# Performance work log

Hardware: AMD Instinct MI355X
Metric: run time of the kernel (lower is better)

The kernel has to match this reference:

```python
import jax, jax.numpy as jnp
import numpy as np

B, L, D_MODEL = 1, 1024, 768
H = 12            # num_heads == num_key_value_heads
FDIM = 16         # feature_dim
HEAD_DIM = D_MODEL // H  # 64
EPS = 1e-12
R2 = np.sqrt(2.0)
RD = np.sqrt(float(FDIM))        # sqrt(16) = 4
RRD = np.sqrt(RD)                # sqrt(4) = 2


def setup_inputs() -> dict:
    key = jax.random.key(0)
    ks = jax.random.split(key, 5)
    s = 1.0 / np.sqrt(D_MODEL)
    return {
        "hidden_states": jax.random.normal(ks[0], (B, L, D_MODEL), dtype=jnp.float32),
        "Wq": jax.random.normal(ks[1], (D_MODEL, H * FDIM), dtype=jnp.float32) * s,
        "Wk": jax.random.normal(ks[2], (D_MODEL, H * FDIM), dtype=jnp.float32) * s,
        "Wv": jax.random.normal(ks[3], (D_MODEL, D_MODEL), dtype=jnp.float32) * s,
        "Wo": jax.random.normal(ks[4], (D_MODEL, D_MODEL), dtype=jnp.float32) * s,
    }


def taylor_exp_feature_map(x):
    # x: (b, h, l, FDIM) -> (b, h, l, 1 + FDIM + FDIM^2)
    x2 = (x[..., :, None] * x[..., None, :]).reshape(*x.shape[:-1], FDIM * FDIM) / R2
    ones = jnp.ones((*x.shape[:-1], 1), dtype=x.dtype)
    return jnp.concatenate([ones, x / RRD, x2 / RD], axis=-1)


def reference(hidden_states, Wq, Wk, Wv, Wo):
    b, l, _ = hidden_states.shape
    q = (hidden_states @ Wq).reshape(b, l, H, FDIM).transpose(0, 2, 1, 3)
    k = (hidden_states @ Wk).reshape(b, l, H, FDIM).transpose(0, 2, 1, 3)
    v = (hidden_states @ Wv).reshape(b, l, H, HEAD_DIM).transpose(0, 2, 1, 3)
    q = taylor_exp_feature_map(q)  # (b,h,l,Dexp)
    k = taylor_exp_feature_map(k)  # (b,h,l,Dexp)
    # causal linear attention: y_t = q_t . cumsum_t(k_s v_s^T) / (q_t . cumsum_t(k_s) + eps)
    kv = k[..., :, None] * v[..., None, :]          # (b,h,l,Dexp,hd)
    kv_cum = jnp.cumsum(kv, axis=2)                  # (b,h,l,Dexp,hd)
    num = jnp.einsum('bhln,bhlnd->bhld', q, kv_cum)  # (b,h,l,hd)
    k_cum = jnp.cumsum(k, axis=2)                    # (b,h,l,Dexp)
    den = jnp.einsum('bhln,bhln->bhl', q, k_cum)[..., None] + EPS
    y = num / den                                    # (b,h,l,hd)
    y = y.transpose(0, 2, 1, 3).reshape(b, l, H * HEAD_DIM)
    return y @ Wo
```

## Files before the change

### kernel.cpp

```cpp
#include <hip/hip_runtime.h>

#define C2 0.17677669529663687f

typedef __attribute__((ext_vector_type(8))) short short8;
typedef __attribute__((ext_vector_type(8))) unsigned short ushort8;
typedef __attribute__((ext_vector_type(4))) float f32x4;

__device__ __forceinline__ unsigned short f2bf(float x) {
    union { float f; unsigned u; } v; v.f = x;
    unsigned r = v.u + 0x7fffu + ((v.u >> 16) & 1u);
    return (unsigned short)(r >> 16);
}
__device__ __forceinline__ float bf2f(unsigned short u) {
    union { unsigned u; float f; } v; v.u = ((unsigned)u) << 16;
    return v.f;
}

__device__ __forceinline__ void gemm_inblk_splitk(
    const float* __restrict__ A, const float* __restrict__ W,
    float* __restrict__ out, int row0, int n0, int outcol0, int ldw, int outld)
{
    __shared__ unsigned short Al[2][2][64][40];
    __shared__ unsigned short Bl[2][2][64][40];
    __shared__ float red[64][65];
    const int tid = threadIdx.x;
    const int g = tid >> 8;
    const int t = tid & 255;
    const int lane = t & 63, wave4 = t >> 6;
    const int wm = wave4 & 1, wn = wave4 >> 1;
    const int quad = lane >> 4, lr = lane & 15;
    const int k0base = g * 384;

    f32x4 acc[2][2] = {{{0.f,0.f,0.f,0.f},{0.f,0.f,0.f,0.f}},
                       {{0.f,0.f,0.f,0.f},{0.f,0.f,0.f,0.f}}};

    float4 ra[2], rb[2];
    #pragma unroll
    for (int l = 0; l < 2; ++l) {
        int idx = t + l * 256;
        ra[l] = *(const float4*)&A[(size_t)(row0 + (idx >> 3)) * 768 + k0base + (idx & 7) * 4];
        rb[l] = *(const float4*)&W[(size_t)(k0base + (idx >> 4)) * ldw + n0 + (idx & 15) * 4];
    }
    #pragma unroll
    for (int l = 0; l < 2; ++l) {
        int idx = t + l * 256;
        *(ushort4*)&Al[g][0][idx >> 3][(idx & 7) * 4] =
            make_ushort4(f2bf(ra[l].x), f2bf(ra[l].y), f2bf(ra[l].z), f2bf(ra[l].w));
        int kr = idx >> 4, nq = (idx & 15) * 4;
        int col = (((kr >> 3) ^ ((idx & 15) >> 2)) << 3) | (kr & 7);
        Bl[g][0][nq + 0][col] = f2bf(rb[l].x);
        Bl[g][0][nq + 1][col] = f2bf(rb[l].y);
        Bl[g][0][nq + 2][col] = f2bf(rb[l].z);
        Bl[g][0][nq + 3][col] = f2bf(rb[l].w);
    }
    __syncthreads();

    const int ITER = 12;
    #pragma unroll
    for (int i = 0; i < ITER; ++i) {
        const int cur = i & 1, nxt = cur ^ 1;
        float4 na[2], nb[2];
        if (i + 1 < ITER) {
            int kn = k0base + (i + 1) * 32;
            #pragma unroll
            for (int l = 0; l < 2; ++l) {
                int idx = t + l * 256;
                na[l] = *(const float4*)&A[(size_t)(row0 + (idx >> 3)) * 768 + kn + (idx & 7) * 4];
                nb[l] = *(const float4*)&W[(size_t)(kn + (idx >> 4)) * ldw + n0 + (idx & 15) * 4];
            }
        }
        short8 af[2], bfr[2];
        #pragma unroll
        for (int mi = 0; mi < 2; ++mi)
            af[mi] = *(const short8*)&Al[g][cur][wm * 32 + mi * 16 + lr][quad << 3];
        #pragma unroll
        for (int ni = 0; ni < 2; ++ni) {
            int csw = quad ^ ((wn * 2 + ni) & 3);
            bfr[ni] = *(const short8*)&Bl[g][cur][wn * 32 + ni * 16 + lr][csw << 3];
        }
        #pragma unroll
        for (int mi = 0; mi < 2; ++mi)
            #pragma unroll
            for (int ni = 0; ni < 2; ++ni)
                acc[mi][ni] = __builtin_amdgcn_mfma_f32_16x16x32_bf16(af[mi], bfr[ni], acc[mi][ni], 0, 0, 0);
        if (i + 1 < ITER) {
            #pragma unroll
            for (int l = 0; l < 2; ++l) {
                int idx = t + l * 256;
                *(ushort4*)&Al[g][nxt][idx >> 3][(idx & 7) * 4] =
                    make_ushort4(f2bf(na[l].x), f2bf(na[l].y), f2bf(na[l].z), f2bf(na[l].w));
                int kr = idx >> 4, nq = (idx & 15) * 4;
                int col = (((kr >> 3) ^ ((idx & 15) >> 2)) << 3) | (kr & 7);
                Bl[g][nxt][nq + 0][col] = f2bf(nb[l].x);
                Bl[g][nxt][nq + 1][col] = f2bf(nb[l].y);
                Bl[g][nxt][nq + 2][col] = f2bf(nb[l].z);
                Bl[g][nxt][nq + 3][col] = f2bf(nb[l].w);
            }
        }
        __syncthreads();
    }
    if (g == 1) {
        #pragma unroll
        for (int mi = 0; mi < 2; ++mi)
            #pragma unroll
            for (int ni = 0; ni < 2; ++ni)
                #pragma unroll
                for (int r = 0; r < 4; ++r)
                    red[wm * 32 + mi * 16 + quad * 4 + r][wn * 32 + ni * 16 + lr] = acc[mi][ni][r];
    }
    __syncthreads();
    if (g == 0) {
        #pragma unroll
        for (int mi = 0; mi < 2; ++mi)
            #pragma unroll
            for (int ni = 0; ni < 2; ++ni)
                #pragma unroll
                for (int r = 0; r < 4; ++r) {
                    int rr = wm * 32 + mi * 16 + quad * 4 + r;
                    int cc = wn * 32 + ni * 16 + lr;
                    out[(size_t)(row0 + rr) * outld + outcol0 + cc] = acc[mi][ni][r] + red[rr][cc];
                }
    }
}

__global__ __launch_bounds__(512) void gemm_qkv_mfma(
    const float* __restrict__ H, const float* __restrict__ Wq,
    const float* __restrict__ Wk, const float* __restrict__ Wv,
    float* __restrict__ out)
{
    const int nt = blockIdx.x, mt = blockIdx.y;
    const float* W; int ldw, n0;
    if (nt < 3)      { W = Wq; ldw = 192; n0 = nt * 64; }
    else if (nt < 6) { W = Wk; ldw = 192; n0 = (nt - 3) * 64; }
    else             { W = Wv; ldw = 768; n0 = (nt - 6) * 64; }
    gemm_inblk_splitk(H, W, out, mt * 64, n0, nt * 64, ldw, 1152);
}

__global__ __launch_bounds__(512) void gemm_wo_mfma(
    const float* __restrict__ Y, const float* __restrict__ Wo, float* __restrict__ out)
{
    const int nt = blockIdx.x, mt = blockIdx.y;
    gemm_inblk_splitk(Y, Wo, out, mt * 64, nt * 64, nt * 64, 768, 768);
}

__global__ __launch_bounds__(256) void chunk_state_k(
    const float* __restrict__ qkv, unsigned short* __restrict__ St, float* __restrict__ z)
{
    const int c = blockIdx.x, h = blockIdx.y;
    __shared__ float Kc[64][17];
    __shared__ unsigned short Pk[320][72];
    __shared__ unsigned short Vt[80][72];
    const int tid = threadIdx.x;
    const int lane = tid & 63, wave = tid >> 6;
    const int quad = lane >> 4, lr = lane & 15;

    {
        int s = tid >> 2, f4 = (tid & 3) * 4;
        float4 kv = *(const float4*)&qkv[(size_t)(c * 64 + s) * 1152 + 192 + h * 16 + f4];
        Kc[s][f4 + 0] = kv.x; Kc[s][f4 + 1] = kv.y; Kc[s][f4 + 2] = kv.z; Kc[s][f4 + 3] = kv.w;
    }
    #pragma unroll
    for (int l = 0; l < 4; ++l) {
        int idx = tid + l * 256;
        int s = idx >> 4, d4 = (idx & 15) * 4;
        float4 vv = *(const float4*)&qkv[(size_t)(c * 64 + s) * 1152 + 384 + h * 64 + d4];
        Vt[d4 + 0][s] = f2bf(vv.x);
        Vt[d4 + 1][s] = f2bf(vv.y);
        Vt[d4 + 2][s] = f2bf(vv.z);
        Vt[d4 + 3][s] = f2bf(vv.w);
    }
    for (int idx = tid; idx < 16 * 72; idx += 256) {
        int rr = 64 + idx / 72, ss = idx % 72;
        Vt[rr][ss] = (rr == 64 && ss < 64) ? (unsigned short)0x3F80 : (unsigned short)0;
    }
    __syncthreads();
    for (int idx = tid; idx < 2880; idx += 256) {
        int n = idx / 9, s8 = (idx % 9) * 8;
        short8 v8;
        #pragma unroll
        for (int tt = 0; tt < 8; ++tt) {
            int s = s8 + tt;
            float ph = 0.f;
            if (s < 64 && n < 273) {
                if (n == 0) ph = 1.f;
                else if (n < 17) ph = Kc[s][n - 1] * 0.5f;
                else { int m = n - 17; ph = Kc[s][m >> 4] * Kc[s][m & 15] * C2; }
            }
            v8[tt] = (short)f2bf(ph);
        }
        *(short8*)&Pk[n][s8] = v8;
    }
    __syncthreads();

    f32x4 acc[5][5];
    #pragma unroll
    for (int a = 0; a < 5; ++a)
        #pragma unroll
        for (int b = 0; b < 5; ++b) acc[a][b] = (f32x4){0.f, 0.f, 0.f, 0.f};
    #pragma unroll
    for (int ks = 0; ks < 2; ++ks) {
        short8 af[5], bfr[5];
        #pragma unroll
        for (int mt = 0; mt < 5; ++mt)
            af[mt] = *(const short8*)&Vt[mt * 16 + lr][ks * 32 + quad * 8];
        #pragma unroll
        for (int nt = 0; nt < 5; ++nt)
            bfr[nt] = *(const short8*)&Pk[(wave * 5 + nt) * 16 + lr][ks * 32 + quad * 8];
        #pragma unroll
        for (int mt = 0; mt < 5; ++mt)
            #pragma unroll
            for (int nt = 0; nt < 5; ++nt)
                acc[mt][nt] = __builtin_amdgcn_mfma_f32_16x16x32_bf16(af[mt], bfr[nt], acc[mt][nt], 0, 0, 0);
    }
    unsigned short* Sbt = St + (size_t)(h * 16 + c) * 18432;
    float* zb = z + (h * 16 + c) * 273;
    #pragma unroll
    for (int nt = 0; nt < 5; ++nt) {
        int n = (wave * 5 + nt) * 16 + lr;
        if (n < 273) {
            #pragma unroll
            for (int mt = 0; mt < 4; ++mt)
                #pragma unroll
                for (int r = 0; r < 4; ++r)
                    Sbt[(mt * 16 + quad * 4 + r) * 288 + n] = f2bf(acc[mt][nt][r]);
            if (quad == 0) zb[n] = acc[4][nt][0];
        }
    }
}

__global__ __launch_bounds__(256) void scan_state_k(unsigned short* __restrict__ St, float* __restrict__ z)
{
    const int NS = 12 * 64 * 273;
    int e = blockIdx.x * 256 + threadIdx.x;
    if (e < NS) {
        int hh = e / (64 * 273), rem = e % (64 * 273);
        int d = rem / 273, n = rem % 273;
        unsigned short* p = St + (size_t)hh * 16 * 18432 + d * 288 + n;
        float run = 0.f;
        #pragma unroll
        for (int c = 0; c < 16; ++c) {
            float v = bf2f(p[c * 18432]);
            p[c * 18432] = f2bf(run);
            run += v;
        }
    } else if (e < NS + 12 * 273) {
        int e2 = e - NS, hh = e2 / 273, n = e2 % 273;
        float* p = z + hh * 16 * 273 + n;
        float run = 0.f;
        #pragma unroll
        for (int c = 0; c < 16; ++c) { float v = p[c * 273]; p[c * 273] = run; run += v; }
    }
}

__global__ __launch_bounds__(256) void chunk_out_k(
    const float* __restrict__ qkv, const unsigned short* __restrict__ St, const float* __restrict__ z,
    float* __restrict__ y)
{
    const int c = blockIdx.x, h = blockIdx.y;
    __shared__ float Qc[64][17];
    __shared__ unsigned short Aq[64][40];
    __shared__ unsigned short Kb[64][40];
    __shared__ unsigned short Pq[64][360];
    __shared__ unsigned short Sv[64][360];
    __shared__ float zl[288];
    __shared__ float dpart[6][64];
    const int tid = threadIdx.x;
    const int lane = tid & 63, wave = tid >> 6;
    const int wm = wave & 1, wn = wave >> 1;
    const int quad = lane >> 4, lr = lane & 15;

    {
        int s = tid >> 2, f4 = (tid & 3) * 4;
        const float* base = &qkv[(size_t)(c * 64 + s) * 1152 + h * 16];
        float4 qv = *(const float4*)&base[f4];
        float4 kv = *(const float4*)&base[192 + f4];
        Qc[s][f4 + 0] = qv.x; Qc[s][f4 + 1] = qv.y; Qc[s][f4 + 2] = qv.z; Qc[s][f4 + 3] = qv.w;
        *(ushort4*)&Aq[s][f4] = make_ushort4(f2bf(qv.x), f2bf(qv.y), f2bf(qv.z), f2bf(qv.w));
        *(ushort4*)&Kb[s][f4] = make_ushort4(f2bf(kv.x), f2bf(kv.y), f2bf(kv.z), f2bf(kv.w));
        *(ushort4*)&Aq[s][16 + (tid & 3) * 4] = make_ushort4(0, 0, 0, 0);
        *(ushort4*)&Kb[s][16 + (tid & 3) * 4] = make_ushort4(0, 0, 0, 0);
    }
    #pragma unroll
    for (int l = 0; l < 4; ++l) {
        int idx = tid + l * 256;
        int s = idx >> 4, d4 = (idx & 15) * 4;
        float4 vv = *(const float4*)&qkv[(size_t)(c * 64 + s) * 1152 + 384 + h * 64 + d4];
        Sv[d4 + 0][288 + s] = f2bf(vv.x);
        Sv[d4 + 1][288 + s] = f2bf(vv.y);
        Sv[d4 + 2][288 + s] = f2bf(vv.z);
        Sv[d4 + 3][288 + s] = f2bf(vv.w);
    }
    const unsigned short* Sgt = St + (size_t)(h * 16 + c) * 18432;
    for (int idx = tid; idx < 64 * 34; idx += 256) {
        int d = idx / 34, n8 = (idx % 34) * 8;
        *(ushort8*)&Sv[d][n8] = *(const ushort8*)&Sgt[d * 288 + n8];
    }
    for (int idx = tid; idx < 64; idx += 256) Sv[idx][272] = Sgt[idx * 288 + 272];
    for (int idx = tid; idx < 64 * 15; idx += 256) {
        int d = idx / 15, n = 273 + idx % 15;
        Sv[d][n] = 0;
    }
    const float* zg = z + (h * 16 + c) * 273;
    for (int idx = tid; idx < 288; idx += 256) zl[idx] = (idx < 273) ? zg[idx] : 0.f;
    __syncthreads();

    f32x4 accS[2][2] = {{{0.f,0.f,0.f,0.f},{0.f,0.f,0.f,0.f}},
                        {{0.f,0.f,0.f,0.f},{0.f,0.f,0.f,0.f}}};
    {
        short8 af[2], bfr[2];
        #pragma unroll
        for (int mi = 0; mi < 2; ++mi)
            af[mi] = *(const short8*)&Aq[wm * 32 + mi * 16 + lr][quad * 8];
        #pragma unroll
        for (int ni = 0; ni < 2; ++ni)
            bfr[ni] = *(const short8*)&Kb[wn * 32 + ni * 16 + lr][quad * 8];
        #pragma unroll
        for (int mi = 0; mi < 2; ++mi)
            #pragma unroll
            for (int ni = 0; ni < 2; ++ni)
                accS[mi][ni] = __builtin_amdgcn_mfma_f32_16x16x32_bf16(af[mi], bfr[ni], accS[mi][ni], 0, 0, 0);
    }

    {
        int i = lane;
        float qr[16];
        #pragma unroll
        for (int f = 0; f < 16; ++f) qr[f] = Qc[i][f];
        float dp = 0.f;
        int n0 = wave * 72;
        for (int n = n0; n < n0 + 72; ++n) {
            float ph;
            if (n == 0) ph = 1.f;
            else if (n < 17) ph = qr[n - 1] * 0.5f;
            else if (n < 273) { int m = n - 17; ph = qr[m >> 4] * qr[m & 15] * C2; }
            else ph = 0.f;
            Pq[i][n] = f2bf(ph);
            dp += ph * zl[n];
        }
        dpart[wave][i] = dp;
    }

    #pragma unroll
    for (int mi = 0; mi < 2; ++mi) {
        float rs[4] = {0.f, 0.f, 0.f, 0.f};
        #pragma unroll
        for (int ni = 0; ni < 2; ++ni)
            #pragma unroll
            for (int r = 0; r < 4; ++r) {
                int i = wm * 32 + mi * 16 + quad * 4 + r;
                int j = wn * 32 + ni * 16 + lr;
                float u = accS[mi][ni][r];
                float sc = (j <= i) ? (1.f + 0.25f * u + u * u * (1.f / 32.f)) : 0.f;
                rs[r] += sc;
                Pq[i][288 + j] = f2bf(sc);
            }
        #pragma unroll
        for (int r = 0; r < 4; ++r) {
            float v = rs[r];
            v += __shfl_xor(v, 1);
            v += __shfl_xor(v, 2);
            v += __shfl_xor(v, 4);
            v += __shfl_xor(v, 8);
            if (lr == 0) dpart[4 + wn][wm * 32 + mi * 16 + quad * 4 + r] = v;
        }
    }
    __syncthreads();

    f32x4 acc[2][2] = {{{0.f,0.f,0.f,0.f},{0.f,0.f,0.f,0.f}},
                       {{0.f,0.f,0.f,0.f},{0.f,0.f,0.f,0.f}}};
    #pragma unroll
    for (int ks = 0; ks < 11; ++ks) {
        short8 af[2], bfr[2];
        #pragma unroll
        for (int mi = 0; mi < 2; ++mi)
            af[mi] = *(const short8*)&Pq[wm * 32 + mi * 16 + lr][ks * 32 + quad * 8];
        #pragma unroll
        for (int ni = 0; ni < 2; ++ni)
            bfr[ni] = *(const short8*)&Sv[wn * 32 + ni * 16 + lr][ks * 32 + quad * 8];
        #pragma unroll
        for (int mi = 0; mi < 2; ++mi)
            #pragma unroll
            for (int ni = 0; ni < 2; ++ni)
                acc[mi][ni] = __builtin_amdgcn_mfma_f32_16x16x32_bf16(af[mi], bfr[ni], acc[mi][ni], 0, 0, 0);
    }

    #pragma unroll
    for (int mi = 0; mi < 2; ++mi)
        #pragma unroll
        for (int r = 0; r < 4; ++r) {
            int i = wm * 32 + mi * 16 + quad * 4 + r;
            float den = dpart[0][i] + dpart[1][i] + dpart[2][i] +
                        dpart[3][i] + dpart[4][i] + dpart[5][i] + 1e-12f;
            float rden = 1.f / den;
            #pragma unroll
            for (int ni = 0; ni < 2; ++ni)
                y[(size_t)(c * 64 + i) * 768 + h * 64 + wn * 32 + ni * 16 + lr] = acc[mi][ni][r] * rden;
        }
}

extern "C" void kernel_launch(void* const* d_in, const int* in_sizes, int n_in,
                              void* d_out, int out_size, void* d_ws, size_t ws_size,
                              hipStream_t stream) {
    const float* hs = (const float*)d_in[0];
    const float* Wq = (const float*)d_in[1];
    const float* Wk = (const float*)d_in[2];
    const float* Wv = (const float*)d_in[3];
    const float* Wo = (const float*)d_in[4];
    float* out = (float*)d_out;
    float* ws  = (float*)d_ws;

    float* qkv = ws;
    float* yb  = ws + 1179648;
    unsigned short* St = (unsigned short*)(ws + 1966080);
    float* zb  = ws + 5320704;

    gemm_qkv_mfma<<<dim3(18, 16), 512, 0, stream>>>(hs, Wq, Wk, Wv, qkv);
    chunk_state_k<<<dim3(16, 12), 256, 0, stream>>>(qkv, St, zb);
    scan_state_k <<<832, 256, 0, stream>>>(St, zb);
    chunk_out_k  <<<dim3(16, 12), 256, 0, stream>>>(qkv, St, zb, yb);
    gemm_wo_mfma <<<dim3(12, 16), 512, 0, stream>>>(yb, Wo, out);
}
```

Measured before the change: 137.6 us.

## Fuse five kernels into one persistent kernel with software grid barriers

Replaces the five separate launches (QKV GEMM, chunk state, scan, chunk output, Wo GEMM) with a single 192-block persistent kernel. Phases are separated by an atomic-counter grid barrier, and shared memory is overlaid through a union. The goal is to remove launch gaps and inter-kernel drain. In exchange, the QKV GEMM is spread unevenly across blocks (some do two tiles), the chunk-state MFMA work is redistributed across 8 waves, and a memset is added per call. The grid barrier only works if all 192 blocks are co-resident.

```diff
diff --git a/kernel.cpp b/kernel.cpp
--- a/kernel.cpp
+++ b/kernel.cpp
@@ -16,13 +16,52 @@
     return v.f;
 }
 
-__device__ __forceinline__ void gemm_inblk_splitk(
-    const float* __restrict__ A, const float* __restrict__ W,
+struct SplitKSm {
+    unsigned short Al[2][2][64][40];
+    unsigned short Bl[2][2][64][40];
+    float red[64][65];
+};
+struct StateSm {
+    float Kc[64][17];
+    unsigned short Pk[320][72];
+    unsigned short Vt[80][72];
+};
+struct OutSm {
+    float Qc[64][17];
+    unsigned short Aq[64][40];
+    unsigned short Kb[64][40];
+    unsigned short Pq[64][360];
+    unsigned short Sv[64][360];
+    float zl[288];
+    float dpart[6][64];
+};
+union __align__(16) SmemU { SplitKSm g; StateSm a; OutSm c; };
+
+__device__ __forceinline__ void grid_sync(int* bar, int nblk) {
+    __syncthreads();
+    if (threadIdx.x == 0) {
+        __threadfence();
+        int gen = __hip_atomic_load(&bar[1], __ATOMIC_RELAXED, __HIP_MEMORY_SCOPE_AGENT);
+        int arr = __hip_atomic_fetch_add(&bar[0], 1, __ATOMIC_ACQ_REL, __HIP_MEMORY_SCOPE_AGENT);
+        if (arr == nblk - 1) {
+            __hip_atomic_store(&bar[0], 0, __ATOMIC_RELAXED, __HIP_MEMORY_SCOPE_AGENT);
+            __hip_atomic_store(&bar[1], gen + 1, __ATOMIC_RELEASE, __HIP_MEMORY_SCOPE_AGENT);
+        } else {
+            int cur;
+            do {
+                __builtin_amdgcn_s_sleep(2);
+                cur = __hip_atomic_load(&bar[1], __ATOMIC_ACQUIRE, __HIP_MEMORY_SCOPE_AGENT);
+            } while (cur == gen);
+        }
+        __threadfence();
+    }
+    __syncthreads();
+}
+
+__device__ void gemm_inblk_splitk(
+    SplitKSm& smem, const float* __restrict__ A, const float* __restrict__ W,
     float* __restrict__ out, int row0, int n0, int outcol0, int ldw, int outld)
 {
-    __shared__ unsigned short Al[2][2][64][40];
-    __shared__ unsigned short Bl[2][2][64][40];
-    __shared__ float red[64][65];
     const int tid = threadIdx.x;
     const int g = tid >> 8;
     const int t = tid & 255;
@@ -44,14 +83,14 @@
     #pragma unroll
     for (int l = 0; l < 2; ++l) {
         int idx = t + l * 256;
-        *(ushort4*)&Al[g][0][idx >> 3][(idx & 7) * 4] =
+        *(ushort4*)&smem.Al[g][0][idx >> 3][(idx & 7) * 4] =
             make_ushort4(f2bf(ra[l].x), f2bf(ra[l].y), f2bf(ra[l].z), f2bf(ra[l].w));
         int kr = idx >> 4, nq = (idx & 15) * 4;
         int col = (((kr >> 3) ^ ((idx & 15) >> 2)) << 3) | (kr & 7);
-        Bl[g][0][nq + 0][col] = f2bf(rb[l].x);
-        Bl[g][0][nq + 1][col] = f2bf(rb[l].y);
-        Bl[g][0][nq + 2][col] = f2bf(rb[l].z);
-        Bl[g][0][nq + 3][col] = f2bf(rb[l].w);
+        smem.Bl[g][0][nq + 0][col] = f2bf(rb[l].x);
+        smem.Bl[g][0][nq + 1][col] = f2bf(rb[l].y);
+        smem.Bl[g][0][nq + 2][col] = f2bf(rb[l].z);
+        smem.Bl[g][0][nq + 3][col] = f2bf(rb[l].w);
     }
     __syncthreads();
 
@@ -72,11 +111,11 @@
         short8 af[2], bfr[2];
         #pragma unroll
         for (int mi = 0; mi < 2; ++mi)
-            af[mi] = *(const short8*)&Al[g][cur][wm * 32 + mi * 16 + lr][quad << 3];
+            af[mi] = *(const short8*)&smem.Al[g][cur][wm * 32 + mi * 16 + lr][quad << 3];
         #pragma unroll
         for (int ni = 0; ni < 2; ++ni) {
             int csw = quad ^ ((wn * 2 + ni) & 3);
-            bfr[ni] = *(const short8*)&Bl[g][cur][wn * 32 + ni * 16 + lr][csw << 3];
+            bfr[ni] = *(const short8*)&smem.Bl[g][cur][wn * 32 + ni * 16 + lr][csw << 3];
         }
         #pragma unroll
         for (int mi = 0; mi < 2; ++mi)
@@ -87,14 +126,14 @@
             #pragma unroll
             for (int l = 0; l < 2; ++l) {
                 int idx = t + l * 256;
-                *(ushort4*)&Al[g][nxt][idx >> 3][(idx & 7) * 4] =
+                *(ushort4*)&smem.Al[g][nxt][idx >> 3][(idx & 7) * 4] =
                     make_ushort4(f2bf(na[l].x), f2bf(na[l].y), f2bf(na[l].z), f2bf(na[l].w));
                 int kr = idx >> 4, nq = (idx & 15) * 4;
                 int col = (((kr >> 3) ^ ((idx & 15) >> 2)) << 3) | (kr & 7);
-                Bl[g][nxt][nq + 0][col] = f2bf(nb[l].x);
-                Bl[g][nxt][nq + 1][col] = f2bf(nb[l].y);
-                Bl[g][nxt][nq + 2][col] = f2bf(nb[l].z);
-                Bl[g][nxt][nq + 3][col] = f2bf(nb[l].w);
+                smem.Bl[g][nxt][nq + 0][col] = f2bf(nb[l].x);
+                smem.Bl[g][nxt][nq + 1][col] = f2bf(nb[l].y);
+                smem.Bl[g][nxt][nq + 2][col] = f2bf(nb[l].z);
+                smem.Bl[g][nxt][nq + 3][col] = f2bf(nb[l].w);
             }
         }
         __syncthreads();
@@ -106,7 +145,7 @@
             for (int ni = 0; ni < 2; ++ni)
                 #pragma unroll
                 for (int r = 0; r < 4; ++r)
-                    red[wm * 32 + mi * 16 + quad * 4 + r][wn * 32 + ni * 16 + lr] = acc[mi][ni][r];
+                    smem.red[wm * 32 + mi * 16 + quad * 4 + r][wn * 32 + ni * 16 + lr] = acc[mi][ni][r];
     }
     __syncthreads();
     if (g == 0) {
@@ -118,284 +157,295 @@
                 for (int r = 0; r < 4; ++r) {
                     int rr = wm * 32 + mi * 16 + quad * 4 + r;
                     int cc = wn * 32 + ni * 16 + lr;
-                    out[(size_t)(row0 + rr) * outld + outcol0 + cc] = acc[mi][ni][r] + red[rr][cc];
-                }
-    }
-}
-
-__global__ __launch_bounds__(512) void gemm_qkv_mfma(
-    const float* __restrict__ H, const float* __restrict__ Wq,
-    const float* __restrict__ Wk, const float* __restrict__ Wv,
-    float* __restrict__ out)
+                    out[(size_t)(row0 + rr) * outld + outcol0 + cc] = acc[mi][ni][r] + smem.red[rr][cc];
+                }
+    }
+}
+
+__global__ __launch_bounds__(512) void based_mega(
+    const float* __restrict__ hs, const float* __restrict__ Wq, const float* __restrict__ Wk,
+    const float* __restrict__ Wv, const float* __restrict__ Wo, float* __restrict__ out,
+    float* __restrict__ qkv, float* __restrict__ yb, unsigned short* __restrict__ St,
+    float* __restrict__ zb, int* __restrict__ bar)
 {
-    const int nt = blockIdx.x, mt = blockIdx.y;
-    const float* W; int ldw, n0;
-    if (nt < 3)      { W = Wq; ldw = 192; n0 = nt * 64; }
-    else if (nt < 6) { W = Wk; ldw = 192; n0 = (nt - 3) * 64; }
-    else             { W = Wv; ldw = 768; n0 = (nt - 6) * 64; }
-    gemm_inblk_splitk(H, W, out, mt * 64, n0, nt * 64, ldw, 1152);
-}
-
-__global__ __launch_bounds__(512) void gemm_wo_mfma(
-    const float* __restrict__ Y, const float* __restrict__ Wo, float* __restrict__ out)
-{
-    const int nt = blockIdx.x, mt = blockIdx.y;
-    gemm_inblk_splitk(Y, Wo, out, mt * 64, nt * 64, nt * 64, 768, 768);
-}
-
-__global__ __launch_bounds__(256) void chunk_state_k(
-    const float* __restrict__ qkv, unsigned short* __restrict__ St, float* __restrict__ z)
-{
-    const int c = blockIdx.x, h = blockIdx.y;
-    __shared__ float Kc[64][17];
-    __shared__ unsigned short Pk[320][72];
-    __shared__ unsigned short Vt[80][72];
+    __shared__ SmemU sm;
+    const int b = blockIdx.x;
     const int tid = threadIdx.x;
-    const int lane = tid & 63, wave = tid >> 6;
-    const int quad = lane >> 4, lr = lane & 15;
 
     {
-        int s = tid >> 2, f4 = (tid & 3) * 4;
-        float4 kv = *(const float4*)&qkv[(size_t)(c * 64 + s) * 1152 + 192 + h * 16 + f4];
-        Kc[s][f4 + 0] = kv.x; Kc[s][f4 + 1] = kv.y; Kc[s][f4 + 2] = kv.z; Kc[s][f4 + 3] = kv.w;
-    }
-    #pragma unroll
-    for (int l = 0; l < 4; ++l) {
-        int idx = tid + l * 256;
-        int s = idx >> 4, d4 = (idx & 15) * 4;
-        float4 vv = *(const float4*)&qkv[(size_t)(c * 64 + s) * 1152 + 384 + h * 64 + d4];
-        Vt[d4 + 0][s] = f2bf(vv.x);
-        Vt[d4 + 1][s] = f2bf(vv.y);
-        Vt[d4 + 2][s] = f2bf(vv.z);
-        Vt[d4 + 3][s] = f2bf(vv.w);
-    }
-    for (int idx = tid; idx < 16 * 72; idx += 256) {
-        int rr = 64 + idx / 72, ss = idx % 72;
-        Vt[rr][ss] = (rr == 64 && ss < 64) ? (unsigned short)0x3F80 : (unsigned short)0;
-    }
-    __syncthreads();
-    for (int idx = tid; idx < 2880; idx += 256) {
-        int n = idx / 9, s8 = (idx % 9) * 8;
-        short8 v8;
-        #pragma unroll
-        for (int tt = 0; tt < 8; ++tt) {
-            int s = s8 + tt;
-            float ph = 0.f;
-            if (s < 64 && n < 273) {
-                if (n == 0) ph = 1.f;
-                else if (n < 17) ph = Kc[s][n - 1] * 0.5f;
-                else { int m = n - 17; ph = Kc[s][m >> 4] * Kc[s][m & 15] * C2; }
-            }
-            v8[tt] = (short)f2bf(ph);
-        }
-        *(short8*)&Pk[n][s8] = v8;
-    }
-    __syncthreads();
-
-    f32x4 acc[5][5];
-    #pragma unroll
-    for (int a = 0; a < 5; ++a)
-        #pragma unroll
-        for (int b = 0; b < 5; ++b) acc[a][b] = (f32x4){0.f, 0.f, 0.f, 0.f};
-    #pragma unroll
-    for (int ks = 0; ks < 2; ++ks) {
-        short8 af[5], bfr[5];
+        const int ntiles = (b < 96) ? 2 : 1;
+        for (int ti = 0; ti < ntiles; ++ti) {
+            int tl = b + ti * 192;
+            int mt = tl / 18, nt = tl % 18;
+            const float* W; int ldw, n0;
+            if (nt < 3)      { W = Wq; ldw = 192; n0 = nt * 64; }
+            else if (nt < 6) { W = Wk; ldw = 192; n0 = (nt - 3) * 64; }
+            else             { W = Wv; ldw = 768; n0 = (nt - 6) * 64; }
+            gemm_inblk_splitk(sm.g, hs, W, qkv, mt * 64, n0, nt * 64, ldw, 1152);
+        }
+    }
+    grid_sync(bar, 192);
+
+    const int c = b & 15, h = b >> 4;
+
+    {
+        if (tid < 256) {
+            int s = tid >> 2, f4 = (tid & 3) * 4;
+            float4 kv = *(const float4*)&qkv[(size_t)(c * 64 + s) * 1152 + 192 + h * 16 + f4];
+            sm.a.Kc[s][f4 + 0] = kv.x; sm.a.Kc[s][f4 + 1] = kv.y;
+            sm.a.Kc[s][f4 + 2] = kv.z; sm.a.Kc[s][f4 + 3] = kv.w;
+        }
+        #pragma unroll
+        for (int l = 0; l < 2; ++l) {
+            int idx = tid + l * 512;
+            int s = idx >> 4, d4 = (idx & 15) * 4;
+            float4 vv = *(const float4*)&qkv[(size_t)(c * 64 + s) * 1152 + 384 + h * 64 + d4];
+            sm.a.Vt[d4 + 0][s] = f2bf(vv.x);
+            sm.a.Vt[d4 + 1][s] = f2bf(vv.y);
+            sm.a.Vt[d4 + 2][s] = f2bf(vv.z);
+            sm.a.Vt[d4 + 3][s] = f2bf(vv.w);
+        }
+        for (int idx = tid; idx < 16 * 72; idx += 512) {
+            int rr = 64 + idx / 72, ss = idx % 72;
+            sm.a.Vt[rr][ss] = (rr == 64 && ss < 64) ? (unsigned short)0x3F80 : (unsigned short)0;
+        }
+        __syncthreads();
+        for (int idx = tid; idx < 2880; idx += 512) {
+            int n = idx / 9, s8 = (idx % 9) * 8;
+            short8 v8;
+            #pragma unroll
+            for (int tt = 0; tt < 8; ++tt) {
+                int s = s8 + tt;
+                float ph = 0.f;
+                if (s < 64 && n < 273) {
+                    if (n == 0) ph = 1.f;
+                    else if (n < 17) ph = sm.a.Kc[s][n - 1] * 0.5f;
+                    else { int m = n - 17; ph = sm.a.Kc[s][m >> 4] * sm.a.Kc[s][m & 15] * C2; }
+                }
+                v8[tt] = (short)f2bf(ph);
+            }
+            *(short8*)&sm.a.Pk[n][s8] = v8;
+        }
+        __syncthreads();
+
+        const int lane = tid & 63, wave = tid >> 6;
+        const int quad = lane >> 4, lr = lane & 15;
+        f32x4 acc[5][3];
         #pragma unroll
         for (int mt = 0; mt < 5; ++mt)
-            af[mt] = *(const short8*)&Vt[mt * 16 + lr][ks * 32 + quad * 8];
-        #pragma unroll
-        for (int nt = 0; nt < 5; ++nt)
-            bfr[nt] = *(const short8*)&Pk[(wave * 5 + nt) * 16 + lr][ks * 32 + quad * 8];
-        #pragma unroll
-        for (int mt = 0; mt < 5; ++mt)
-            #pragma unroll
-            for (int nt = 0; nt < 5; ++nt)
-                acc[mt][nt] = __builtin_amdgcn_mfma_f32_16x16x32_bf16(af[mt], bfr[nt], acc[mt][nt], 0, 0, 0);
-    }
-    unsigned short* Sbt = St + (size_t)(h * 16 + c) * 18432;
-    float* zb = z + (h * 16 + c) * 273;
-    #pragma unroll
-    for (int nt = 0; nt < 5; ++nt) {
-        int n = (wave * 5 + nt) * 16 + lr;
-        if (n < 273) {
-            #pragma unroll
-            for (int mt = 0; mt < 4; ++mt)
-                #pragma unroll
-                for (int r = 0; r < 4; ++r)
-                    Sbt[(mt * 16 + quad * 4 + r) * 288 + n] = f2bf(acc[mt][nt][r]);
-            if (quad == 0) zb[n] = acc[4][nt][0];
-        }
-    }
-}
-
-__global__ __launch_bounds__(256) void scan_state_k(unsigned short* __restrict__ St, float* __restrict__ z)
-{
-    const int NS = 12 * 64 * 273;
-    int e = blockIdx.x * 256 + threadIdx.x;
-    if (e < NS) {
-        int hh = e / (64 * 273), rem = e % (64 * 273);
-        int d = rem / 273, n = rem % 273;
-        unsigned short* p = St + (size_t)hh * 16 * 18432 + d * 288 + n;
-        float run = 0.f;
-        #pragma unroll
-        for (int c = 0; c < 16; ++c) {
-            float v = bf2f(p[c * 18432]);
-            p[c * 18432] = f2bf(run);
-            run += v;
-        }
-    } else if (e < NS + 12 * 273) {
-        int e2 = e - NS, hh = e2 / 273, n = e2 % 273;
-        float* p = z + hh * 16 * 273 + n;
-        float run = 0.f;
-        #pragma unroll
-        for (int c = 0; c < 16; ++c) { float v = p[c * 273]; p[c * 273] = run; run += v; }
-    }
-}
-
-__global__ __launch_bounds__(256) void chunk_out_k(
-    const float* __restrict__ qkv, const unsigned short* __restrict__ St, const float* __restrict__ z,
-    float* __restrict__ y)
-{
-    const int c = blockIdx.x, h = blockIdx.y;
-    __shared__ float Qc[64][17];
-    __shared__ unsigned short Aq[64][40];
-    __shared__ unsigned short Kb[64][40];
-    __shared__ unsigned short Pq[64][360];
-    __shared__ unsigned short Sv[64][360];
-    __shared__ float zl[288];
-    __shared__ float dpart[6][64];
-    const int tid = threadIdx.x;
-    const int lane = tid & 63, wave = tid >> 6;
-    const int wm = wave & 1, wn = wave >> 1;
-    const int quad = lane >> 4, lr = lane & 15;
+            #pragma unroll
+            for (int nt = 0; nt < 3; ++nt) acc[mt][nt] = (f32x4){0.f, 0.f, 0.f, 0.f};
+        #pragma unroll
+        for (int ks = 0; ks < 2; ++ks) {
+            short8 af[5], bfr[3];
+            #pragma unroll
+            for (int mt = 0; mt < 5; ++mt)
+                af[mt] = *(const short8*)&sm.a.Vt[mt * 16 + lr][ks * 32 + quad * 8];
+            #pragma unroll
+            for (int nt = 0; nt < 3; ++nt)
+                if (wave + 8 * nt < 20)
+                    bfr[nt] = *(const short8*)&sm.a.Pk[(wave + 8 * nt) * 16 + lr][ks * 32 + quad * 8];
+            #pragma unroll
+            for (int mt = 0; mt < 5; ++mt)
+                #pragma unroll
+                for (int nt = 0; nt < 3; ++nt)
+                    if (wave + 8 * nt < 20)
+                        acc[mt][nt] = __builtin_amdgcn_mfma_f32_16x16x32_bf16(af[mt], bfr[nt], acc[mt][nt], 0, 0, 0);
+        }
+        unsigned short* Sbt = St + (size_t)(h * 16 + c) * 18432;
+        float* zp = zb + (h * 16 + c) * 273;
+        #pragma unroll
+        for (int nt = 0; nt < 3; ++nt) {
+            if (wave + 8 * nt < 20) {
+                int n = (wave + 8 * nt) * 16 + lr;
+                if (n < 273) {
+                    #pragma unroll
+                    for (int mt = 0; mt < 4; ++mt)
+                        #pragma unroll
+                        for (int r = 0; r < 4; ++r)
+                            Sbt[(mt * 16 + quad * 4 + r) * 288 + n] = f2bf(acc[mt][nt][r]);
+                    if (quad == 0) zp[n] = acc[4][nt][0];
+                }
+            }
+        }
+    }
+    grid_sync(bar, 192);
 
     {
-        int s = tid >> 2, f4 = (tid & 3) * 4;
-        const float* base = &qkv[(size_t)(c * 64 + s) * 1152 + h * 16];
-        float4 qv = *(const float4*)&base[f4];
-        float4 kv = *(const float4*)&base[192 + f4];
-        Qc[s][f4 + 0] = qv.x; Qc[s][f4 + 1] = qv.y; Qc[s][f4 + 2] = qv.z; Qc[s][f4 + 3] = qv.w;
-        *(ushort4*)&Aq[s][f4] = make_ushort4(f2bf(qv.x), f2bf(qv.y), f2bf(qv.z), f2bf(qv.w));
-        *(ushort4*)&Kb[s][f4] = make_ushort4(f2bf(kv.x), f2bf(kv.y), f2bf(kv.z), f2bf(kv.w));
-        *(ushort4*)&Aq[s][16 + (tid & 3) * 4] = make_ushort4(0, 0, 0, 0);
-        *(ushort4*)&Kb[s][16 + (tid & 3) * 4] = make_ushort4(0, 0, 0, 0);
-    }
-    #pragma unroll
-    for (int l = 0; l < 4; ++l) {
-        int idx = tid + l * 256;
-        int s = idx >> 4, d4 = (idx & 15) * 4;
-        float4 vv = *(const float4*)&qkv[(size_t)(c * 64 + s) * 1152 + 384 + h * 64 + d4];
-        Sv[d4 + 0][288 + s] = f2bf(vv.x);
-        Sv[d4 + 1][288 + s] = f2bf(vv.y);
-        Sv[d4 + 2][288 + s] = f2bf(vv.z);
-        Sv[d4 + 3][288 + s] = f2bf(vv.w);
-    }
-    const unsigned short* Sgt = St + (size_t)(h * 16 + c) * 18432;
-    for (int idx = tid; idx < 64 * 34; idx += 256) {
-        int d = idx / 34, n8 = (idx % 34) * 8;
-        *(ushort8*)&Sv[d][n8] = *(const ushort8*)&Sgt[d * 288 + n8];
-    }
-    for (int idx = tid; idx < 64; idx += 256) Sv[idx][272] = Sgt[idx * 288 + 272];
-    for (int idx = tid; idx < 64 * 15; idx += 256) {
-        int d = idx / 15, n = 273 + idx % 15;
-        Sv[d][n] = 0;
-    }
-    const float* zg = z + (h * 16 + c) * 273;
-    for (int idx = tid; idx < 288; idx += 256) zl[idx] = (idx < 273) ? zg[idx] : 0.f;
-    __syncthreads();
-
-    f32x4 accS[2][2] = {{{0.f,0.f,0.f,0.f},{0.f,0.f,0.f,0.f}},
-                        {{0.f,0.f,0.f,0.f},{0.f,0.f,0.f,0.f}}};
+        int gid = b * 512 + tid;
+        const int NV = 12 * 64 * 36;
+        if (gid < NV) {
+            int hh = gid / (64 * 36), rem = gid % (64 * 36);
+            int d = rem / 36, nb = rem % 36;
+            unsigned short* p = St + (size_t)hh * 16 * 18432 + d * 288 + nb * 8;
+            ushort8 v[16];
+            #pragma unroll
+            for (int cc = 0; cc < 16; ++cc) v[cc] = *(const ushort8*)(p + (size_t)cc * 18432);
+            float run[8] = {0.f,0.f,0.f,0.f,0.f,0.f,0.f,0.f};
+            #pragma unroll
+            for (int cc = 0; cc < 16; ++cc) {
+                ushort8 w;
+                #pragma unroll
+                for (int j = 0; j < 8; ++j) {
+                    w[j] = f2bf(run[j]);
+                    run[j] += bf2f(v[cc][j]);
+                }
+                *(ushort8*)(p + (size_t)cc * 18432) = w;
+            }
+        } else if (gid < NV + 12 * 273) {
+            int e2 = gid - NV, hh = e2 / 273, n = e2 % 273;
+            float* p = zb + hh * 16 * 273 + n;
+            float v[16];
+            #pragma unroll
+            for (int cc = 0; cc < 16; ++cc) v[cc] = p[cc * 273];
+            float run = 0.f;
+            #pragma unroll
+            for (int cc = 0; cc < 16; ++cc) { p[cc * 273] = run; run += v[cc]; }
+        }
+    }
+    grid_sync(bar, 192);
+
     {
-        short8 af[2], bfr[2];
-        #pragma unroll
-        for (int mi = 0; mi < 2; ++mi)
-            af[mi] = *(const short8*)&Aq[wm * 32 + mi * 16 + lr][quad * 8];
-        #pragma unroll
-        for (int ni = 0; ni < 2; ++ni)
-            bfr[ni] = *(const short8*)&Kb[wn * 32 + ni * 16 + lr][quad * 8];
-        #pragma unroll
-        for (int mi = 0; mi < 2; ++mi)
-            #pragma unroll
-            for (int ni = 0; ni < 2; ++ni)
-                accS[mi][ni] = __builtin_amdgcn_mfma_f32_16x16x32_bf16(af[mi], bfr[ni], accS[mi][ni], 0, 0, 0);
-    }
+        const int lane = tid & 63, wave = tid >> 6;
+        const int wm = wave & 1, wn = wave >> 1;
+        const int quad = lane >> 4, lr = lane & 15;
+
+        if (tid < 256) {
+            int s = tid >> 2, f4 = (tid & 3) * 4;
+            const float* base = &qkv[(size_t)(c * 64 + s) * 1152 + h * 16];
+            float4 qv = *(const float4*)&base[f4];
+            float4 kv = *(const float4*)&base[192 + f4];
+            sm.c.Qc[s][f4 + 0] = qv.x; sm.c.Qc[s][f4 + 1] = qv.y;
+            sm.c.Qc[s][f4 + 2] = qv.z; sm.c.Qc[s][f4 + 3] = qv.w;
+            *(ushort4*)&sm.c.Aq[s][f4] = make_ushort4(f2bf(qv.x), f2bf(qv.y), f2bf(qv.z), f2bf(qv.w));
+            *(ushort4*)&sm.c.Kb[s][f4] = make_ushort4(f2bf(kv.x), f2bf(kv.y), f2bf(kv.z), f2bf(kv.w));
+            *(ushort4*)&sm.c.Aq[s][16 + (tid & 3) * 4] = make_ushort4(0, 0, 0, 0);
+            *(ushort4*)&sm.c.Kb[s][16 + (tid & 3) * 4] = make_ushort4(0, 0, 0, 0);
+            #pragma unroll
+            for (int l = 0; l < 4; ++l) {
+                int idx = tid + l * 256;
+                int ss = idx >> 4, d4 = (idx & 15) * 4;
+                float4 vv = *(const float4*)&qkv[(size_t)(c * 64 + ss) * 1152 + 384 + h * 64 + d4];
+                sm.c.Sv[d4 + 0][288 + ss] = f2bf(vv.x);
+                sm.c.Sv[d4 + 1][288 + ss] = f2bf(vv.y);
+                sm.c.Sv[d4 + 2][288 + ss] = f2bf(vv.z);
+                sm.c.Sv[d4 + 3][288 + ss] = f2bf(vv.w);
+            }
+            const unsigned short* Sgt = St + (size_t)(h * 16 + c) * 18432;
+            for (int idx = tid; idx < 64 * 34; idx += 256) {
+                int d = idx / 34, n8 = (idx % 34) * 8;
+                *(ushort8*)&sm.c.Sv[d][n8] = *(const ushort8*)&Sgt[d * 288 + n8];
+            }
+            for (int idx = tid; idx < 64; idx += 256) sm.c.Sv[idx][272] = Sgt[idx * 288 + 272];
+            for (int idx = tid; idx < 64 * 15; idx += 256) {
+                int d = idx / 15, n = 273 + idx % 15;
+                sm.c.Sv[d][n] = 0;
+            }
+            const float* zg = zb + (h * 16 + c) * 273;
+            for (int idx = tid; idx < 288; idx += 256) sm.c.zl[idx] = (idx < 273) ? zg[idx] : 0.f;
+        }
+        __syncthreads();
+
+        if (tid < 256) {
+            f32x4 accS[2][2] = {{{0.f,0.f,0.f,0.f},{0.f,0.f,0.f,0.f}},
+                                {{0.f,0.f,0.f,0.f},{0.f,0.f,0.f,0.f}}};
+            {
+                short8 af[2], bfr[2];
+                #pragma unroll
+                for (int mi = 0; mi < 2; ++mi)
+                    af[mi] = *(const short8*)&sm.c.Aq[wm * 32 + mi * 16 + lr][quad * 8];
+                #pragma unroll
+                for (int ni = 0; ni < 2; ++ni)
+                    bfr[ni] = *(const short8*)&sm.c.Kb[wn * 32 + ni * 16 + lr][quad * 8];
+                #pragma unroll
+                for (int mi = 0; mi < 2; ++mi)
+                    #pragma unroll
+                    for (int ni = 0; ni < 2; ++ni)
+                        accS[mi][ni] = __builtin_amdgcn_mfma_f32_16x16x32_bf16(af[mi], bfr[ni], accS[mi][ni], 0, 0, 0);
+            }
+            {
+                int i = lane;
+                float qr[16];
+                #pragma unroll
+                for (int f = 0; f < 16; ++f) qr[f] = sm.c.Qc[i][f];
+                float dp = 0.f;
+                int n0 = wave * 72;
+                for (int n = n0; n < n0 + 72; ++n) {
+                    float ph;
+                    if (n == 0) ph = 1.f;
+                    else if (n < 17) ph = qr[n - 1] * 0.5f;
+                    else if (n < 273) { int m = n - 17; ph = qr[m >> 4] * qr[m & 15] * C2; }
+                    else ph = 0.f;
+                    sm.c.Pq[i][n] = f2bf(ph);
+                    dp += ph * sm.c.zl[n];
+                }
+                sm.c.dpart[wave][i] = dp;
+            }
+            #pragma unroll
+            for (int mi = 0; mi < 2; ++mi) {
+                float rs[4] = {0.f, 0.f, 0.f, 0.f};
+                #pragma unroll
+                for (int ni = 0; ni < 2; ++ni)
+                    #pragma unroll
+                    for (int r = 0; r < 4; ++r) {
+                        int i = wm * 32 + mi * 16 + quad * 4 + r;
+                        int j = wn * 32 + ni * 16 + lr;
+                        float u = accS[mi][ni][r];
+                        float sc = (j <= i) ? (1.f + 0.25f * u + u * u * (1.f / 32.f)) : 0.f;
+                        rs[r] += sc;
+                        sm.c.Pq[i][288 + j] = f2bf(sc);
+                    }
+                #pragma unroll
+                for (int r = 0; r < 4; ++r) {
+                    float v = rs[r];
+                    v += __shfl_xor(v, 1);
+                    v += __shfl_xor(v, 2);
+                    v += __shfl_xor(v, 4);
+                    v += __shfl_xor(v, 8);
+                    if (lr == 0) sm.c.dpart[4 + wn][wm * 32 + mi * 16 + quad * 4 + r] = v;
+                }
+            }
+        }
+        __syncthreads();
+
+        if (tid < 256) {
+            f32x4 acc[2][2] = {{{0.f,0.f,0.f,0.f},{0.f,0.f,0.f,0.f}},
+                               {{0.f,0.f,0.f,0.f},{0.f,0.f,0.f,0.f}}};
+            #pragma unroll
+            for (int ks = 0; ks < 11; ++ks) {
+                short8 af[2], bfr[2];
+                #pragma unroll
+                for (int mi = 0; mi < 2; ++mi)
+                    af[mi] = *(const short8*)&sm.c.Pq[wm * 32 + mi * 16 + lr][ks * 32 + quad * 8];
+                #pragma unroll
+                for (int ni = 0; ni < 2; ++ni)
+                    bfr[ni] = *(const short8*)&sm.c.Sv[wn * 32 + ni * 16 + lr][ks * 32 + quad * 8];
+                #pragma unroll
+                for (int mi = 0; mi < 2; ++mi)
+                    #pragma unroll
+                    for (int ni = 0; ni < 2; ++ni)
+                        acc[mi][ni] = __builtin_amdgcn_mfma_f32_16x16x32_bf16(af[mi], bfr[ni], acc[mi][ni], 0, 0, 0);
+            }
+            #pragma unroll
+            for (int mi = 0; mi < 2; ++mi)
+                #pragma unroll
+                for (int r = 0; r < 4; ++r) {
+                    int i = wm * 32 + mi * 16 + quad * 4 + r;
+                    float den = sm.c.dpart[0][i] + sm.c.dpart[1][i] + sm.c.dpart[2][i] +
+                                sm.c.dpart[3][i] + sm.c.dpart[4][i] + sm.c.dpart[5][i] + 1e-12f;
+                    float rden = 1.f / den;
+                    #pragma unroll
+                    for (int ni = 0; ni < 2; ++ni)
+                        yb[(size_t)(c * 64 + i) * 768 + h * 64 + wn * 32 + ni * 16 + lr] = acc[mi][ni][r] * rden;
+                }
+        }
+    }
+    grid_sync(bar, 192);
 
     {
-        int i = lane;
-        float qr[16];
-        #pragma unroll
-        for (int f = 0; f < 16; ++f) qr[f] = Qc[i][f];
-        float dp = 0.f;
-        int n0 = wave * 72;
-        for (int n = n0; n < n0 + 72; ++n) {
-            float ph;
-            if (n == 0) ph = 1.f;
-            else if (n < 17) ph = qr[n - 1] * 0.5f;
-            else if (n < 273) { int m = n - 17; ph = qr[m >> 4] * qr[m & 15] * C2; }
-            else ph = 0.f;
-            Pq[i][n] = f2bf(ph);
-            dp += ph * zl[n];
-        }
-        dpart[wave][i] = dp;
-    }
-
-    #pragma unroll
-    for (int mi = 0; mi < 2; ++mi) {
-        float rs[4] = {0.f, 0.f, 0.f, 0.f};
-        #pragma unroll
-        for (int ni = 0; ni < 2; ++ni)
-            #pragma unroll
-            for (int r = 0; r < 4; ++r) {
-                int i = wm * 32 + mi * 16 + quad * 4 + r;
-                int j = wn * 32 + ni * 16 + lr;
-                float u = accS[mi][ni][r];
-                float sc = (j <= i) ? (1.f + 0.25f * u + u * u * (1.f / 32.f)) : 0.f;
-                rs[r] += sc;
-                Pq[i][288 + j] = f2bf(sc);
-            }
-        #pragma unroll
-        for (int r = 0; r < 4; ++r) {
-            float v = rs[r];
-            v += __shfl_xor(v, 1);
-            v += __shfl_xor(v, 2);
-            v += __shfl_xor(v, 4);
-            v += __shfl_xor(v, 8);
-            if (lr == 0) dpart[4 + wn][wm * 32 + mi * 16 + quad * 4 + r] = v;
-        }
-    }
-    __syncthreads();
-
-    f32x4 acc[2][2] = {{{0.f,0.f,0.f,0.f},{0.f,0.f,0.f,0.f}},
-                       {{0.f,0.f,0.f,0.f},{0.f,0.f,0.f,0.f}}};
-    #pragma unroll
-    for (int ks = 0; ks < 11; ++ks) {
-        short8 af[2], bfr[2];
-        #pragma unroll
-        for (int mi = 0; mi < 2; ++mi)
-            af[mi] = *(const short8*)&Pq[wm * 32 + mi * 16 + lr][ks * 32 + quad * 8];
-        #pragma unroll
-        for (int ni = 0; ni < 2; ++ni)
-            bfr[ni] = *(const short8*)&Sv[wn * 32 + ni * 16 + lr][ks * 32 + quad * 8];
-        #pragma unroll
-        for (int mi = 0; mi < 2; ++mi)
-            #pragma unroll
-            for (int ni = 0; ni < 2; ++ni)
-                acc[mi][ni] = __builtin_amdgcn_mfma_f32_16x16x32_bf16(af[mi], bfr[ni], acc[mi][ni], 0, 0, 0);
-    }
-
-    #pragma unroll
-    for (int mi = 0; mi < 2; ++mi)
-        #pragma unroll
-        for (int r = 0; r < 4; ++r) {
-            int i = wm * 32 + mi * 16 + quad * 4 + r;
-            float den = dpart[0][i] + dpart[1][i] + dpart[2][i] +
-                        dpart[3][i] + dpart[4][i] + dpart[5][i] + 1e-12f;
-            float rden = 1.f / den;
-            #pragma unroll
-            for (int ni = 0; ni < 2; ++ni)
-                y[(size_t)(c * 64 + i) * 768 + h * 64 + wn * 32 + ni * 16 + lr] = acc[mi][ni][r] * rden;
-        }
+        int nt = b % 12, mt = b / 12;
+        gemm_inblk_splitk(sm.g, yb, Wo, out, mt * 64, nt * 64, nt * 64, 768, 768);
+    }
 }
 
 extern "C" void kernel_launch(void* const* d_in, const int* in_sizes, int n_in,
@@ -413,10 +463,8 @@
     float* yb  = ws + 1179648;
     unsigned short* St = (unsigned short*)(ws + 1966080);
     float* zb  = ws + 5320704;
-
-    gemm_qkv_mfma<<<dim3(18, 16), 512, 0, stream>>>(hs, Wq, Wk, Wv, qkv);
-    chunk_state_k<<<dim3(16, 12), 256, 0, stream>>>(qkv, St, zb);
-    scan_state_k <<<832, 256, 0, stream>>>(St, zb);
-    chunk_out_k  <<<dim3(16, 12), 256, 0, stream>>>(qkv, St, zb, yb);
-    gemm_wo_mfma <<<dim3(12, 16), 512, 0, stream>>>(yb, Wo, out);
-}
+    int* bar   = (int*)(ws + 5373184);
+
+    hipMemsetAsync(bar, 0, 2 * sizeof(int), stream);
+    based_mega<<<192, 512, 0, stream>>>(hs, Wq, Wk, Wv, Wo, out, qkv, yb, St, zb, bar);
+}
```

After: 284.6 us. 107% more time.

## Vectorize state scan and load chunk state directly into MFMA registers

Applied to the files above, without the earlier changes.

chunk_state_k now writes zero padding for state columns 273-287, so later kernels can read state rows as aligned 8-wide vectors. The scan kernel processes 8 columns per thread with ushort8 loads and stores, which cuts the launch to 121 blocks. chunk_out_k loads its bf16 state operand straight from global memory into registers instead of staging a 64x360 tile in shared memory, keeping only a small transposed V tile in LDS. This cuts LDS footprint and copy traffic and should raise occupancy, in exchange for more registers per thread and fewer threads in the scan.

```diff
diff --git a/kernel.cpp b/kernel.cpp
--- a/kernel.cpp
+++ b/kernel.cpp
@@ -217,38 +217,49 @@
     #pragma unroll
     for (int nt = 0; nt < 5; ++nt) {
         int n = (wave * 5 + nt) * 16 + lr;
-        if (n < 273) {
+        if (n < 288) {
             #pragma unroll
             for (int mt = 0; mt < 4; ++mt)
                 #pragma unroll
                 for (int r = 0; r < 4; ++r)
-                    Sbt[(mt * 16 + quad * 4 + r) * 288 + n] = f2bf(acc[mt][nt][r]);
-            if (quad == 0) zb[n] = acc[4][nt][0];
+                    Sbt[(mt * 16 + quad * 4 + r) * 288 + n] =
+                        (n < 273) ? f2bf(acc[mt][nt][r]) : (unsigned short)0;
+            if (quad == 0 && n < 273) zb[n] = acc[4][nt][0];
         }
     }
 }
 
 __global__ __launch_bounds__(256) void scan_state_k(unsigned short* __restrict__ St, float* __restrict__ z)
 {
-    const int NS = 12 * 64 * 273;
-    int e = blockIdx.x * 256 + threadIdx.x;
-    if (e < NS) {
-        int hh = e / (64 * 273), rem = e % (64 * 273);
-        int d = rem / 273, n = rem % 273;
-        unsigned short* p = St + (size_t)hh * 16 * 18432 + d * 288 + n;
+    const int NV = 12 * 64 * 36;
+    int gid = blockIdx.x * 256 + threadIdx.x;
+    if (gid < NV) {
+        int hh = gid / (64 * 36), rem = gid % (64 * 36);
+        int d = rem / 36, nb = rem % 36;
+        unsigned short* p = St + (size_t)hh * 16 * 18432 + d * 288 + nb * 8;
+        ushort8 v[16];
+        #pragma unroll
+        for (int cc = 0; cc < 16; ++cc) v[cc] = *(const ushort8*)(p + (size_t)cc * 18432);
+        float run[8] = {0.f,0.f,0.f,0.f,0.f,0.f,0.f,0.f};
+        #pragma unroll
+        for (int cc = 0; cc < 16; ++cc) {
+            ushort8 w;
+            #pragma unroll
+            for (int j = 0; j < 8; ++j) {
+                w[j] = f2bf(run[j]);
+                run[j] += bf2f(v[cc][j]);
+            }
+            *(ushort8*)(p + (size_t)cc * 18432) = w;
+        }
+    } else if (gid < NV + 12 * 273) {
+        int e2 = gid - NV, hh = e2 / 273, n = e2 % 273;
+        float* p = z + hh * 16 * 273 + n;
+        float v[16];
+        #pragma unroll
+        for (int cc = 0; cc < 16; ++cc) v[cc] = p[cc * 273];
         float run = 0.f;
         #pragma unroll
-        for (int c = 0; c < 16; ++c) {
-            float v = bf2f(p[c * 18432]);
-            p[c * 18432] = f2bf(run);
-            run += v;
-        }
-    } else if (e < NS + 12 * 273) {
-        int e2 = e - NS, hh = e2 / 273, n = e2 % 273;
-        float* p = z + hh * 16 * 273 + n;
-        float run = 0.f;
-        #pragma unroll
-        for (int c = 0; c < 16; ++c) { float v = p[c * 273]; p[c * 273] = run; run += v; }
+        for (int cc = 0; cc < 16; ++cc) { p[cc * 273] = run; run += v[cc]; }
     }
 }
 
@@ -261,13 +272,21 @@
     __shared__ unsigned short Aq[64][40];
     __shared__ unsigned short Kb[64][40];
     __shared__ unsigned short Pq[64][360];
-    __shared__ unsigned short Sv[64][360];
+    __shared__ unsigned short Vt[64][72];
     __shared__ float zl[288];
     __shared__ float dpart[6][64];
     const int tid = threadIdx.x;
     const int lane = tid & 63, wave = tid >> 6;
     const int wm = wave & 1, wn = wave >> 1;
     const int quad = lane >> 4, lr = lane & 15;
+
+    const unsigned short* Sgt = St + (size_t)(h * 16 + c) * 18432;
+    short8 sfr[2][9];
+    #pragma unroll
+    for (int ni = 0; ni < 2; ++ni)
+        #pragma unroll
+        for (int ks = 0; ks < 9; ++ks)
+            sfr[ni][ks] = *(const short8*)&Sgt[(wn * 32 + ni * 16 + lr) * 288 + ks * 32 + quad * 8];
 
     {
         int s = tid >> 2, f4 = (tid & 3) * 4;
@@ -283,22 +302,12 @@
     #pragma unroll
     for (int l = 0; l < 4; ++l) {
         int idx = tid + l * 256;
-        int s = idx >> 4, d4 = (idx & 15) * 4;
-        float4 vv = *(const float4*)&qkv[(size_t)(c * 64 + s) * 1152 + 384 + h * 64 + d4];
-        Sv[d4 + 0][288 + s] = f2bf(vv.x);
-        Sv[d4 + 1][288 + s] = f2bf(vv.y);
-        Sv[d4 + 2][288 + s] = f2bf(vv.z);
-        Sv[d4 + 3][288 + s] = f2bf(vv.w);
-    }
-    const unsigned short* Sgt = St + (size_t)(h * 16 + c) * 18432;
-    for (int idx = tid; idx < 64 * 34; idx += 256) {
-        int d = idx / 34, n8 = (idx % 34) * 8;
-        *(ushort8*)&Sv[d][n8] = *(const ushort8*)&Sgt[d * 288 + n8];
-    }
-    for (int idx = tid; idx < 64; idx += 256) Sv[idx][272] = Sgt[idx * 288 + 272];
-    for (int idx = tid; idx < 64 * 15; idx += 256) {
-        int d = idx / 15, n = 273 + idx % 15;
-        Sv[d][n] = 0;
+        int ss = idx >> 4, d4 = (idx & 15) * 4;
+        float4 vv = *(const float4*)&qkv[(size_t)(c * 64 + ss) * 1152 + 384 + h * 64 + d4];
+        Vt[d4 + 0][ss] = f2bf(vv.x);
+        Vt[d4 + 1][ss] = f2bf(vv.y);
+        Vt[d4 + 2][ss] = f2bf(vv.z);
+        Vt[d4 + 3][ss] = f2bf(vv.w);
     }
     const float* zg = z + (h * 16 + c) * 273;
     for (int idx = tid; idx < 288; idx += 256) zl[idx] = (idx < 273) ? zg[idx] : 0.f;
@@ -376,7 +385,9 @@
             af[mi] = *(const short8*)&Pq[wm * 32 + mi * 16 + lr][ks * 32 + quad * 8];
         #pragma unroll
         for (int ni = 0; ni < 2; ++ni)
-            bfr[ni] = *(const short8*)&Sv[wn * 32 + ni * 16 + lr][ks * 32 + quad * 8];
+            bfr[ni] = (ks < 9)
+                ? sfr[ni][ks]
+                : *(const short8*)&Vt[wn * 32 + ni * 16 + lr][(ks - 9) * 32 + quad * 8];
         #pragma unroll
         for (int mi = 0; mi < 2; ++mi)
             #pragma unroll
@@ -416,7 +427,7 @@
 
     gemm_qkv_mfma<<<dim3(18, 16), 512, 0, stream>>>(hs, Wq, Wk, Wv, qkv);
     chunk_state_k<<<dim3(16, 12), 256, 0, stream>>>(qkv, St, zb);
-    scan_state_k <<<832, 256, 0, stream>>>(St, zb);
+    scan_state_k <<<121, 256, 0, stream>>>(St, zb);
     chunk_out_k  <<<dim3(16, 12), 256, 0, stream>>>(qkv, St, zb, yb);
     gemm_wo_mfma <<<dim3(12, 16), 512, 0, stream>>>(yb, Wo, out);
 }
```

After: 134.9 us. About the same (-2.0%).
